# Optimization experiments

Hardware: AMD Instinct MI355X
Metric: run time of the kernel (lower is better)

Reference implementation:

```python
import jax, jax.numpy as jnp
import numpy as np

B, C, H, W = 4, 256, 64, 64
CS = C // 2  # in_channels // scale_factor
EPS = 1e-5


def _conv1x1(x, w, b):
    # x: [B,C,H,W], w: [O,C], b: [O]
    return jnp.einsum('bchw,oc->bohw', x, w) + b[None, :, None, None]


def setup_inputs() -> dict:
    key = jax.random.key(0)
    ks = jax.random.split(key, 12)
    sq, so = 1.0 / np.sqrt(C), 1.0 / np.sqrt(CS)
    inp = {
        'input': jax.random.normal(ks[0], (B, C, H, W), jnp.float32),
        'Wq': jax.random.normal(ks[1], (CS, C), jnp.float32) * sq,
        'bq': jax.random.normal(ks[2], (CS,), jnp.float32) * 0.01,
        'Wk': jax.random.normal(ks[3], (CS, C), jnp.float32) * sq,
        'bk': jax.random.normal(ks[4], (CS,), jnp.float32) * 0.01,
        'Wv': jax.random.normal(ks[5], (CS, C), jnp.float32) * sq,
        'bv': jax.random.normal(ks[6], (CS,), jnp.float32) * 0.01,
        'Wo': jax.random.normal(ks[7], (C, CS), jnp.float32) * so,
        'bo': jax.random.normal(ks[8], (C,), jnp.float32) * 0.01,
        'gamma': 1.0 + 0.1 * jax.random.normal(ks[9], (C,), jnp.float32),
        'beta': 0.1 * jax.random.normal(ks[10], (C,), jnp.float32),
    }
    return inp


def reference(input, Wq, bq, Wk, bk, Wv, bv, Wo, bo, gamma, beta):
    b, c, w, h = input.shape
    n = w * h
    # 1x1-conv projections -> flattened spatial tokens
    q = _conv1x1(input, Wq, bq).reshape(b, CS, n).transpose(0, 2, 1)  # [B,N,CS]
    k = _conv1x1(input, Wk, bk).reshape(b, CS, n)                     # [B,CS,N]
    attn = jax.nn.softmax(jnp.matmul(q, k), axis=-1)                  # [B,N,N]
    v = _conv1x1(input, Wv, bv).reshape(b, CS, n).transpose(0, 2, 1)  # [B,N,CS]
    out = jnp.matmul(attn, v)                                         # [B,N,CS]
    out = out.transpose(0, 2, 1).reshape(b, CS, w, h)
    # output_conv: Conv2d(1x1) -> BatchNorm2d (training-mode batch stats) -> ReLU
    y = _conv1x1(out, Wo, bo)                                         # [B,C,H,W]
    mean = y.mean(axis=(0, 2, 3))
    var = y.var(axis=(0, 2, 3))  # biased, as torch BN normalization
    yn = (y - mean[None, :, None, None]) * jax.lax.rsqrt(var + EPS)[None, :, None, None]
    yn = yn * gamma[None, :, None, None] + beta[None, :, None, None]
    return jax.nn.relu(yn) + input
```

## Files before the change

kernel.cpp:

```cpp
#include <hip/hip_runtime.h>

#define NTOK 4096
#define NCH  256
#define NCS  128
#define NBAT 4

typedef _Float16 f16;
typedef _Float16 f16x8 __attribute__((ext_vector_type(8)));
typedef _Float16 f16x4 __attribute__((ext_vector_type(4)));
typedef __fp16 fp16x2 __attribute__((ext_vector_type(2)));
typedef float f32x16 __attribute__((ext_vector_type(16)));

__device__ __forceinline__ f16 f2h(float f) { return (f16)f; }
__device__ __forceinline__ float h2f(f16 h) { return (float)h; }
__device__ __forceinline__ unsigned short h2s(f16 h) {
  union { f16 h; unsigned short s; } u; u.h = h; return u.s;
}
__device__ __forceinline__ f32x16 mfma32(f16x8 a, f16x8 b, f32x16 c) {
  return __builtin_amdgcn_mfma_f32_32x32x16_f16(a, b, c, 0, 0, 0);
}
__device__ __forceinline__ unsigned pkrtz(float a, float b) {
  union { fp16x2 h; unsigned u; } u;
  u.h = __builtin_amdgcn_cvt_pkrtz(a, b);
  return u.u;
}

__global__ void k_wconv(const float* __restrict__ wq, const float* __restrict__ wk,
                        const float* __restrict__ wv, const float* __restrict__ wo,
                        f16* __restrict__ out) {
  int i = blockIdx.x * 256 + threadIdx.x;
  int seg = i >> 15, off = i & 32767;
  const float* s = (seg == 0) ? wq : (seg == 1) ? wk : (seg == 2) ? wv : wo;
  out[i] = f2h(s[off]);
}

__launch_bounds__(384)
__global__ void k_qkv(const float* __restrict__ x,
                      const f16* __restrict__ wqb, const f16* __restrict__ wkb,
                      const f16* __restrict__ wvb,
                      const float* __restrict__ bq, const float* __restrict__ bk,
                      const float* __restrict__ bv,
                      f16* __restrict__ Qt, f16* __restrict__ Kt, f16* __restrict__ Vc) {
  __shared__ f16 Xs[64][264];
  const int tid = threadIdx.x;
  const int b = blockIdx.y;
  const int t0 = blockIdx.x * 64;
  const int lane = tid & 63, w = tid >> 6;
  {
    for (int cp = w; cp < 128; cp += 6) {
      const float* xp = x + ((size_t)(b * NCH + 2 * cp)) * NTOK + t0 + lane;
      float f0 = xp[0];
      float f1 = xp[NTOK];
      unsigned pk = (unsigned)h2s(f2h(f0)) | ((unsigned)h2s(f2h(f1)) << 16);
      *(unsigned*)&Xs[lane][2 * cp] = pk;
    }
  }
  __syncthreads();
  const int p = w >> 1, th = w & 1;
  const int cc = lane & 31, hi = lane >> 5;
  const f16* wb = (p == 0) ? wqb : (p == 1) ? wkb : wvb;
  const float* bp = (p == 0) ? bq : (p == 1) ? bk : bv;

  f32x16 acc[4];
  #pragma unroll
  for (int nt = 0; nt < 4; nt++)
    #pragma unroll
    for (int i = 0; i < 16; i++) acc[nt][i] = 0.f;
  #pragma unroll
  for (int ks = 0; ks < 16; ks++) {
    f16x8 a = *(const f16x8*)&Xs[th * 32 + cc][ks * 16 + hi * 8];
    #pragma unroll
    for (int nt = 0; nt < 4; nt++) {
      f16x8 bw = *(const f16x8*)(wb + (size_t)(nt * 32 + cc) * NCH + ks * 16 + hi * 8);
      acc[nt] = mfma32(a, bw, acc[nt]);
    }
  }
  if (p < 2) {
    f16* dst = (p == 0) ? Qt : Kt;
    #pragma unroll
    for (int nt = 0; nt < 4; nt++) {
      const int oc = nt * 32 + cc;
      const float bias = bp[oc];
      #pragma unroll
      for (int i = 0; i < 16; i++) {
        int row = (i & 3) + 8 * (i >> 2) + 4 * hi;
        dst[((size_t)b * NTOK + t0 + th * 32 + row) * NCS + oc] = f2h(acc[nt][i] + bias);
      }
    }
  } else {
    #pragma unroll
    for (int nt = 0; nt < 4; nt++) {
      const int oc = nt * 32 + cc;
      const float bias = bp[oc];
      #pragma unroll
      for (int q = 0; q < 4; q++) {
        f16x4 pk;
        #pragma unroll
        for (int j = 0; j < 4; j++) pk[j] = f2h(acc[nt][4 * q + j] + bias);
        *(f16x4*)(Vc + ((size_t)b * NCS + oc) * NTOK + t0 + th * 32 + 8 * q + 4 * hi) = pk;
      }
    }
  }
}

__launch_bounds__(128)
__global__ void k_attn(const f16* __restrict__ Qt, const f16* __restrict__ Kt,
                       const f16* __restrict__ Vc,
                       f16* __restrict__ OP, float* __restrict__ ML, int niter) {
  __shared__ f16 Ks[64][136];
  __shared__ f16 Vs[128][72];
  __shared__ float als[2][32];
  const int tid = threadIdx.x;
  const int b = blockIdx.x & 3, kh = blockIdx.x >> 2, qt = blockIdx.y;
  const int lane = tid & 63, w = tid >> 6, cc = lane & 31, hi = lane >> 5;

  const f16* qp = Qt + ((size_t)b * NTOK + qt * 64 + w * 32 + cc) * NCS + hi * 8;
  f16x8 qf[8];
  #pragma unroll
  for (int ks = 0; ks < 8; ks++) qf[ks] = *(const f16x8*)(qp + ks * 16);

  f32x16 o[4];
  #pragma unroll
  for (int nt = 0; nt < 4; nt++)
    #pragma unroll
    for (int i = 0; i < 16; i++) o[nt][i] = 0.f;
  float m = -1e30f, l = 0.f;

  const int key = tid >> 1, cb = (tid & 1) * 64;
  const int kb0 = kh * niter * 64;

  for (int it = 0; it < niter; it++) {
    const int kb = kb0 + it * 64;
    __syncthreads();
    {
      const f16* kp = Kt + ((size_t)b * NTOK + kb + key) * NCS + cb;
      #pragma unroll
      for (int pp = 0; pp < 8; pp++)
        *(int4*)&Ks[key][cb + pp * 8] = *(const int4*)(kp + pp * 8);
      const f16* vp = Vc + ((size_t)b * NCS + tid) * NTOK + kb;
      #pragma unroll
      for (int pp = 0; pp < 8; pp++)
        *(int4*)&Vs[tid][pp * 8] = *(const int4*)(vp + pp * 8);
    }
    __syncthreads();

    f32x16 s0, s1;
    #pragma unroll
    for (int i = 0; i < 16; i++) { s0[i] = 0.f; s1[i] = 0.f; }
    #pragma unroll
    for (int ks = 0; ks < 8; ks++) {
      f16x8 a0 = *(const f16x8*)&Ks[cc][ks * 16 + hi * 8];
      f16x8 a1 = *(const f16x8*)&Ks[32 + cc][ks * 16 + hi * 8];
      s0 = mfma32(a0, qf[ks], s0);
      s1 = mfma32(a1, qf[ks], s1);
    }
    float pmax = s0[0];
    #pragma unroll
    for (int i = 1; i < 16; i++) pmax = fmaxf(pmax, s0[i]);
    #pragma unroll
    for (int i = 0; i < 16; i++) pmax = fmaxf(pmax, s1[i]);
    pmax = fmaxf(pmax, __shfl_xor(pmax, 32));
    const float mnew = fmaxf(m, pmax);
    const float alpha = __expf(m - mnew);
    float rs = 0.f;
    #pragma unroll
    for (int i = 0; i < 16; i++) { float e = __expf(s0[i] - mnew); s0[i] = e; rs += e; }
    #pragma unroll
    for (int i = 0; i < 16; i++) { float e = __expf(s1[i] - mnew); s1[i] = e; rs += e; }
    rs += __shfl_xor(rs, 32);
    l = l * alpha + rs;
    m = mnew;
    if (hi == 0) als[w][cc] = alpha;

    f16x8 pav[4];
    {
      unsigned Wt[8];
      #pragma unroll
      for (int t = 0; t < 8; t++) Wt[t] = pkrtz(s0[2 * t], s0[2 * t + 1]);
      asm volatile("v_permlane32_swap_b32 %0, %1" : "+v"(Wt[0]), "+v"(Wt[2]));
      asm volatile("v_permlane32_swap_b32 %0, %1" : "+v"(Wt[1]), "+v"(Wt[3]));
      asm volatile("v_permlane32_swap_b32 %0, %1" : "+v"(Wt[4]), "+v"(Wt[6]));
      asm volatile("v_permlane32_swap_b32 %0, %1" : "+v"(Wt[5]), "+v"(Wt[7]));
      union { unsigned u[4]; f16x8 v; } u0, u1;
      #pragma unroll
      for (int t = 0; t < 4; t++) { u0.u[t] = Wt[t]; u1.u[t] = Wt[4 + t]; }
      pav[0] = u0.v; pav[1] = u1.v;
      #pragma unroll
      for (int t = 0; t < 8; t++) Wt[t] = pkrtz(s1[2 * t], s1[2 * t + 1]);
      asm volatile("v_permlane32_swap_b32 %0, %1" : "+v"(Wt[0]), "+v"(Wt[2]));
      asm volatile("v_permlane32_swap_b32 %0, %1" : "+v"(Wt[1]), "+v"(Wt[3]));
      asm volatile("v_permlane32_swap_b32 %0, %1" : "+v"(Wt[4]), "+v"(Wt[6]));
      asm volatile("v_permlane32_swap_b32 %0, %1" : "+v"(Wt[5]), "+v"(Wt[7]));
      #pragma unroll
      for (int t = 0; t < 4; t++) { u0.u[t] = Wt[t]; u1.u[t] = Wt[4 + t]; }
      pav[2] = u0.v; pav[3] = u1.v;
    }

    float ar[16];
    #pragma unroll
    for (int i = 0; i < 16; i++) ar[i] = als[w][(i & 3) + 8 * (i >> 2) + 4 * hi];
    #pragma unroll
    for (int nt = 0; nt < 4; nt++)
      #pragma unroll
      for (int i = 0; i < 16; i++) o[nt][i] *= ar[i];
    #pragma unroll
    for (int ks = 0; ks < 4; ks++) {
      #pragma unroll
      for (int nt = 0; nt < 4; nt++) {
        f16x8 bv = *(const f16x8*)&Vs[nt * 32 + cc][ks * 16 + hi * 8];
        o[nt] = mfma32(pav[ks], bv, o[nt]);
      }
    }
  }
  const size_t obase = (((size_t)kh * NBAT + b) * NTOK + qt * 64 + w * 32);
  if (hi == 0) {
    const size_t mi = obase + cc;
    ML[mi * 2] = m; ML[mi * 2 + 1] = l;
  }
  #pragma unroll
  for (int nt = 0; nt < 4; nt++)
    #pragma unroll
    for (int i = 0; i < 16; i++) {
      int row = (i & 3) + 8 * (i >> 2) + 4 * hi;
      OP[(obase + row) * NCS + nt * 32 + cc] = f2h(o[nt][i]);
    }
}

template <int S>
__global__ void k_comb(const f16* __restrict__ OP, const float* __restrict__ ML,
                       f16* __restrict__ Oa) {
  const int gid = blockIdx.x * 256 + threadIdx.x;
  const int tok = gid >> 4, dg = (gid & 15) * 8;
  const int b = tok >> 12, tn = tok & 4095;
  float mv[S], lv[S];
  float mm = -1e30f;
  #pragma unroll
  for (int s = 0; s < S; s++) {
    const size_t idx = (((size_t)s * NBAT + b) * NTOK + tn);
    mv[s] = ML[idx * 2]; lv[s] = ML[idx * 2 + 1];
    mm = fmaxf(mm, mv[s]);
  }
  float den = 0.f, wsc[S];
  #pragma unroll
  for (int s = 0; s < S; s++) { wsc[s] = __expf(mv[s] - mm); den += wsc[s] * lv[s]; }
  const float inv = 1.f / den;
  float oacc[8];
  #pragma unroll
  for (int j = 0; j < 8; j++) oacc[j] = 0.f;
  #pragma unroll
  for (int s = 0; s < S; s++) {
    const size_t idx = (((size_t)s * NBAT + b) * NTOK + tn);
    int4 v = *(const int4*)(OP + idx * NCS + dg);
    const f16* a = (const f16*)&v;
    #pragma unroll
    for (int j = 0; j < 8; j++) oacc[j] += wsc[s] * h2f(a[j]);
  }
  f16x8 vv;
  #pragma unroll
  for (int j = 0; j < 8; j++) vv[j] = f2h(oacc[j] * inv);
  *(f16x8*)(Oa + ((size_t)b * NTOK + tn) * NCS + dg) = vv;
}

__launch_bounds__(256)
__global__ void k_out(const f16* __restrict__ Oa, const f16* __restrict__ wob,
                      const float* __restrict__ bo,
                      f16* __restrict__ Yb, float* __restrict__ Psum) {
  __shared__ f16 Es[256][72];
  const int tid = threadIdx.x;
  const int b = blockIdx.y, tt = blockIdx.x, t0 = tt * 64;
  const int lane = tid & 63, w = tid >> 6, cc = lane & 31, hi = lane >> 5;
  const int th = w >> 1, oh = w & 1;
  const f16* op = Oa + ((size_t)b * NTOK + t0 + th * 32 + cc) * NCS + hi * 8;
  f16x8 af[8];
  #pragma unroll
  for (int ks = 0; ks < 8; ks++) af[ks] = *(const f16x8*)(op + ks * 16);
  f32x16 acc[4];
  #pragma unroll
  for (int nt = 0; nt < 4; nt++)
    #pragma unroll
    for (int i = 0; i < 16; i++) acc[nt][i] = 0.f;
  #pragma unroll
  for (int ks = 0; ks < 8; ks++)
    #pragma unroll
    for (int nt = 0; nt < 4; nt++) {
      f16x8 bw = *(const f16x8*)(wob + (size_t)(oh * 128 + nt * 32 + cc) * NCS + ks * 16 + hi * 8);
      acc[nt] = mfma32(af[ks], bw, acc[nt]);
    }
  #pragma unroll
  for (int nt = 0; nt < 4; nt++) {
    const int co = oh * 128 + nt * 32 + cc;
    const float bias = bo[co];
    float s = 0.f, sq = 0.f;
    #pragma unroll
    for (int i = 0; i < 16; i++) {
      float v = acc[nt][i] + bias;
      acc[nt][i] = v; s += v; sq += v * v;
    }
    s += __shfl_xor(s, 32); sq += __shfl_xor(sq, 32);
    if (hi == 0) {
      const size_t pi = ((size_t)(b * 64 + tt) * 2 + th) * NCH + co;
      Psum[pi * 2] = s; Psum[pi * 2 + 1] = sq;
    }
    #pragma unroll
    for (int q = 0; q < 4; q++) {
      f16x4 pk;
      #pragma unroll
      for (int j = 0; j < 4; j++) pk[j] = f2h(acc[nt][4 * q + j]);
      *(f16x4*)&Es[co][th * 32 + q * 8 + hi * 4] = pk;
    }
  }
  __syncthreads();
  {
    const f16* er = &Es[tid][0];
    f16* yp = Yb + ((size_t)b * NCH + tid) * NTOK + t0;
    #pragma unroll
    for (int p = 0; p < 8; p++)
      *(int4*)(yp + p * 8) = *(const int4*)(er + p * 8);
  }
}

__global__ void k_stats(const float* __restrict__ Psum, float* __restrict__ St) {
  const int ch = blockIdx.x, tid = threadIdx.x;
  float s = 0.f, sq = 0.f;
  for (int i = tid; i < 512; i += 128) {
    s  += Psum[((size_t)i * NCH + ch) * 2];
    sq += Psum[((size_t)i * NCH + ch) * 2 + 1];
  }
  #pragma unroll
  for (int off = 32; off >= 1; off >>= 1) { s += __shfl_down(s, off); sq += __shfl_down(sq, off); }
  __shared__ float red[4];
  if ((tid & 63) == 0) { red[(tid >> 6) * 2] = s; red[(tid >> 6) * 2 + 1] = sq; }
  __syncthreads();
  if (tid == 0) {
    s = red[0] + red[2]; sq = red[1] + red[3];
    const float mean = s * (1.f / 16384.f);
    const float var = sq * (1.f / 16384.f) - mean * mean;
    St[ch * 2] = mean;
    St[ch * 2 + 1] = 1.f / sqrtf(var + 1e-5f);
  }
}

__global__ void k_final(const f16* __restrict__ Yb, const float* __restrict__ x,
                        const float* __restrict__ St, const float* __restrict__ gamma,
                        const float* __restrict__ beta, float* __restrict__ out) {
  const size_t i = ((size_t)blockIdx.x * 256 + threadIdx.x) * 8;
  const int ch = (int)((i >> 12) & 255);
  const float mean = St[ch * 2], rstd = St[ch * 2 + 1];
  const float sc = gamma[ch] * rstd;
  const float sh = beta[ch] - mean * sc;
  int4 yv = *(const int4*)(Yb + i);
  const f16* ys = (const f16*)&yv;
  const float4 x0 = *(const float4*)(x + i);
  const float4 x1 = *(const float4*)(x + i + 4);
  float4 o0, o1;
  o0.x = fmaxf(h2f(ys[0]) * sc + sh, 0.f) + x0.x;
  o0.y = fmaxf(h2f(ys[1]) * sc + sh, 0.f) + x0.y;
  o0.z = fmaxf(h2f(ys[2]) * sc + sh, 0.f) + x0.z;
  o0.w = fmaxf(h2f(ys[3]) * sc + sh, 0.f) + x0.w;
  o1.x = fmaxf(h2f(ys[4]) * sc + sh, 0.f) + x1.x;
  o1.y = fmaxf(h2f(ys[5]) * sc + sh, 0.f) + x1.y;
  o1.z = fmaxf(h2f(ys[6]) * sc + sh, 0.f) + x1.z;
  o1.w = fmaxf(h2f(ys[7]) * sc + sh, 0.f) + x1.w;
  *(float4*)(out + i) = o0;
  *(float4*)(out + i + 4) = o1;
}

extern "C" void kernel_launch(void* const* d_in, const int* in_sizes, int n_in,
                              void* d_out, int out_size, void* d_ws, size_t ws_size,
                              hipStream_t stream) {
  const float* x     = (const float*)d_in[0];
  const float* Wq    = (const float*)d_in[1];
  const float* bq    = (const float*)d_in[2];
  const float* Wk    = (const float*)d_in[3];
  const float* bk    = (const float*)d_in[4];
  const float* Wv    = (const float*)d_in[5];
  const float* bv    = (const float*)d_in[6];
  const float* Wo    = (const float*)d_in[7];
  const float* bo    = (const float*)d_in[8];
  const float* gamma = (const float*)d_in[9];
  const float* beta  = (const float*)d_in[10];
  float* out = (float*)d_out;
  char* ws = (char*)d_ws;

  const size_t OFF_W  = 0;
  const size_t OFF_QT = 262144;
  const size_t OFF_KT = OFF_QT + 4194304;
  const size_t OFF_VC = OFF_KT + 4194304;
  const size_t OFF_OP = OFF_VC + 4194304;
  const size_t opsz8 = (size_t)8 * NBAT * NTOK * NCS * 2;
  const size_t mlsz8 = (size_t)8 * NBAT * NTOK * 2 * 4;
  const size_t need8 = OFF_OP + opsz8 + mlsz8 + 1048576 + 4096;
  const int SPLIT = (ws_size >= need8) ? 8 : 4;
  const size_t opsz = (size_t)SPLIT * NBAT * NTOK * NCS * 2;
  const size_t mlsz = (size_t)SPLIT * NBAT * NTOK * 2 * 4;
  const size_t OFF_ML = OFF_OP + opsz;
  const size_t OFF_PS = OFF_ML + mlsz;
  const size_t OFF_ST = OFF_PS + 1048576;

  f16* wqb = (f16*)(ws + OFF_W);
  f16* wkb = (f16*)(ws + OFF_W + 65536);
  f16* wvb = (f16*)(ws + OFF_W + 131072);
  f16* wob = (f16*)(ws + OFF_W + 196608);
  f16* Qt  = (f16*)(ws + OFF_QT);
  f16* Kt  = (f16*)(ws + OFF_KT);
  f16* Vc  = (f16*)(ws + OFF_VC);
  f16* OP  = (f16*)(ws + OFF_OP);
  float* ML = (float*)(ws + OFF_ML);
  float* Psum = (float*)(ws + OFF_PS);
  float* St   = (float*)(ws + OFF_ST);
  f16* Yb = (f16*)(ws + OFF_QT);
  f16* Oa = (f16*)(ws + OFF_VC);

  k_wconv<<<512, 256, 0, stream>>>(Wq, Wk, Wv, Wo, wqb);
  k_qkv<<<dim3(64, 4), 384, 0, stream>>>(x, wqb, wkb, wvb, bq, bk, bv, Qt, Kt, Vc);
  k_attn<<<dim3(4 * SPLIT, 64), 128, 0, stream>>>(Qt, Kt, Vc, OP, ML, 64 / SPLIT);
  if (SPLIT == 8) k_comb<8><<<1024, 256, 0, stream>>>(OP, ML, Oa);
  else            k_comb<4><<<1024, 256, 0, stream>>>(OP, ML, Oa);
  k_out<<<dim3(64, 4), 256, 0, stream>>>(Oa, wob, bo, Yb, Psum);
  k_stats<<<256, 128, 0, stream>>>(Psum, St);
  k_final<<<2048, 256, 0, stream>>>(Yb, x, St, gamma, beta, out);
}
```

Measured before the change: 235.9 us.

## Widen attention blocks to 128 queries, skip rescale when max unchanged, retile QKV

The attention kernel now runs 4 waves per block covering 128 query rows. Each K/V tile loaded into shared memory is reused by twice as many queries, which halves global K/V traffic per query, and a launch bound requests more resident blocks. The online softmax uses a tree max reduction and, when no lane's running max grows (checked wave-wide with __all), skips the alpha computation and the rescale of the output accumulators. The QKV projection kernel is retiled to 32 tokens per block with 12 waves, each wave owning one 32-channel output tile, giving more blocks and less register pressure at the cost of redundant weight reads.

Result: slower. 446.3 us (+89.2%).

```diff
diff --git a/kernel.cpp b/kernel.cpp
--- a/kernel.cpp
+++ b/kernel.cpp
@@ -34,87 +34,73 @@
   out[i] = f2h(s[off]);
 }
 
-__launch_bounds__(384)
+__launch_bounds__(768)
 __global__ void k_qkv(const float* __restrict__ x,
                       const f16* __restrict__ wqb, const f16* __restrict__ wkb,
                       const f16* __restrict__ wvb,
                       const float* __restrict__ bq, const float* __restrict__ bk,
                       const float* __restrict__ bv,
                       f16* __restrict__ Qt, f16* __restrict__ Kt, f16* __restrict__ Vc) {
-  __shared__ f16 Xs[64][264];
+  __shared__ f16 Xs[32][264];
   const int tid = threadIdx.x;
   const int b = blockIdx.y;
-  const int t0 = blockIdx.x * 64;
+  const int t0 = blockIdx.x * 32;
+  for (int idx = tid; idx < 4096; idx += 768) {
+    const int tok = idx & 31, cp = idx >> 5;
+    const float* xp = x + ((size_t)(b * NCH + 2 * cp)) * NTOK + t0 + tok;
+    float f0 = xp[0];
+    float f1 = xp[NTOK];
+    unsigned pk = (unsigned)h2s(f2h(f0)) | ((unsigned)h2s(f2h(f1)) << 16);
+    *(unsigned*)&Xs[tok][2 * cp] = pk;
+  }
+  __syncthreads();
   const int lane = tid & 63, w = tid >> 6;
-  {
-    for (int cp = w; cp < 128; cp += 6) {
-      const float* xp = x + ((size_t)(b * NCH + 2 * cp)) * NTOK + t0 + lane;
-      float f0 = xp[0];
-      float f1 = xp[NTOK];
-      unsigned pk = (unsigned)h2s(f2h(f0)) | ((unsigned)h2s(f2h(f1)) << 16);
-      *(unsigned*)&Xs[lane][2 * cp] = pk;
-    }
-  }
-  __syncthreads();
-  const int p = w >> 1, th = w & 1;
+  const int p = w >> 2, nt = w & 3;
   const int cc = lane & 31, hi = lane >> 5;
   const f16* wb = (p == 0) ? wqb : (p == 1) ? wkb : wvb;
   const float* bp = (p == 0) ? bq : (p == 1) ? bk : bv;
 
-  f32x16 acc[4];
-  #pragma unroll
-  for (int nt = 0; nt < 4; nt++)
-    #pragma unroll
-    for (int i = 0; i < 16; i++) acc[nt][i] = 0.f;
+  f32x16 acc;
+  #pragma unroll
+  for (int i = 0; i < 16; i++) acc[i] = 0.f;
   #pragma unroll
   for (int ks = 0; ks < 16; ks++) {
-    f16x8 a = *(const f16x8*)&Xs[th * 32 + cc][ks * 16 + hi * 8];
-    #pragma unroll
-    for (int nt = 0; nt < 4; nt++) {
-      f16x8 bw = *(const f16x8*)(wb + (size_t)(nt * 32 + cc) * NCH + ks * 16 + hi * 8);
-      acc[nt] = mfma32(a, bw, acc[nt]);
-    }
-  }
+    f16x8 a = *(const f16x8*)&Xs[cc][ks * 16 + hi * 8];
+    f16x8 bw = *(const f16x8*)(wb + (size_t)(nt * 32 + cc) * NCH + ks * 16 + hi * 8);
+    acc = mfma32(a, bw, acc);
+  }
+  const int oc = nt * 32 + cc;
+  const float bias = bp[oc];
   if (p < 2) {
     f16* dst = (p == 0) ? Qt : Kt;
     #pragma unroll
-    for (int nt = 0; nt < 4; nt++) {
-      const int oc = nt * 32 + cc;
-      const float bias = bp[oc];
-      #pragma unroll
-      for (int i = 0; i < 16; i++) {
-        int row = (i & 3) + 8 * (i >> 2) + 4 * hi;
-        dst[((size_t)b * NTOK + t0 + th * 32 + row) * NCS + oc] = f2h(acc[nt][i] + bias);
-      }
+    for (int i = 0; i < 16; i++) {
+      int row = (i & 3) + 8 * (i >> 2) + 4 * hi;
+      dst[((size_t)b * NTOK + t0 + row) * NCS + oc] = f2h(acc[i] + bias);
     }
   } else {
     #pragma unroll
-    for (int nt = 0; nt < 4; nt++) {
-      const int oc = nt * 32 + cc;
-      const float bias = bp[oc];
-      #pragma unroll
-      for (int q = 0; q < 4; q++) {
-        f16x4 pk;
-        #pragma unroll
-        for (int j = 0; j < 4; j++) pk[j] = f2h(acc[nt][4 * q + j] + bias);
-        *(f16x4*)(Vc + ((size_t)b * NCS + oc) * NTOK + t0 + th * 32 + 8 * q + 4 * hi) = pk;
-      }
-    }
-  }
-}
-
-__launch_bounds__(128)
+    for (int q = 0; q < 4; q++) {
+      f16x4 pk;
+      #pragma unroll
+      for (int j = 0; j < 4; j++) pk[j] = f2h(acc[4 * q + j] + bias);
+      *(f16x4*)(Vc + ((size_t)b * NCS + oc) * NTOK + t0 + 8 * q + 4 * hi) = pk;
+    }
+  }
+}
+
+__launch_bounds__(256, 4)
 __global__ void k_attn(const f16* __restrict__ Qt, const f16* __restrict__ Kt,
                        const f16* __restrict__ Vc,
                        f16* __restrict__ OP, float* __restrict__ ML, int niter) {
   __shared__ f16 Ks[64][136];
   __shared__ f16 Vs[128][72];
-  __shared__ float als[2][32];
+  __shared__ float als[4][32];
   const int tid = threadIdx.x;
   const int b = blockIdx.x & 3, kh = blockIdx.x >> 2, qt = blockIdx.y;
   const int lane = tid & 63, w = tid >> 6, cc = lane & 31, hi = lane >> 5;
 
-  const f16* qp = Qt + ((size_t)b * NTOK + qt * 64 + w * 32 + cc) * NCS + hi * 8;
+  const f16* qp = Qt + ((size_t)b * NTOK + qt * 128 + w * 32 + cc) * NCS + hi * 8;
   f16x8 qf[8];
   #pragma unroll
   for (int ks = 0; ks < 8; ks++) qf[ks] = *(const f16x8*)(qp + ks * 16);
@@ -126,21 +112,22 @@
     for (int i = 0; i < 16; i++) o[nt][i] = 0.f;
   float m = -1e30f, l = 0.f;
 
-  const int key = tid >> 1, cb = (tid & 1) * 64;
+  const int kkey = tid >> 2, kcb = (tid & 3) * 32;
+  const int vd = tid >> 1, vh = (tid & 1) * 32;
   const int kb0 = kh * niter * 64;
 
   for (int it = 0; it < niter; it++) {
     const int kb = kb0 + it * 64;
     __syncthreads();
     {
-      const f16* kp = Kt + ((size_t)b * NTOK + kb + key) * NCS + cb;
-      #pragma unroll
-      for (int pp = 0; pp < 8; pp++)
-        *(int4*)&Ks[key][cb + pp * 8] = *(const int4*)(kp + pp * 8);
-      const f16* vp = Vc + ((size_t)b * NCS + tid) * NTOK + kb;
-      #pragma unroll
-      for (int pp = 0; pp < 8; pp++)
-        *(int4*)&Vs[tid][pp * 8] = *(const int4*)(vp + pp * 8);
+      const f16* kp = Kt + ((size_t)b * NTOK + kb + kkey) * NCS + kcb;
+      #pragma unroll
+      for (int pp = 0; pp < 4; pp++)
+        *(int4*)&Ks[kkey][kcb + pp * 8] = *(const int4*)(kp + pp * 8);
+      const f16* vp = Vc + ((size_t)b * NCS + vd) * NTOK + kb + vh;
+      #pragma unroll
+      for (int pp = 0; pp < 4; pp++)
+        *(int4*)&Vs[vd][vh + pp * 8] = *(const int4*)(vp + pp * 8);
     }
     __syncthreads();
 
@@ -154,55 +141,68 @@
       s0 = mfma32(a0, qf[ks], s0);
       s1 = mfma32(a1, qf[ks], s1);
     }
-    float pmax = s0[0];
-    #pragma unroll
-    for (int i = 1; i < 16; i++) pmax = fmaxf(pmax, s0[i]);
-    #pragma unroll
-    for (int i = 0; i < 16; i++) pmax = fmaxf(pmax, s1[i]);
-    pmax = fmaxf(pmax, __shfl_xor(pmax, 32));
-    const float mnew = fmaxf(m, pmax);
-    const float alpha = __expf(m - mnew);
-    float rs = 0.f;
-    #pragma unroll
-    for (int i = 0; i < 16; i++) { float e = __expf(s0[i] - mnew); s0[i] = e; rs += e; }
-    #pragma unroll
-    for (int i = 0; i < 16; i++) { float e = __expf(s1[i] - mnew); s1[i] = e; rs += e; }
-    rs += __shfl_xor(rs, 32);
-    l = l * alpha + rs;
-    m = mnew;
-    if (hi == 0) als[w][cc] = alpha;
+    float t[16];
+    #pragma unroll
+    for (int i = 0; i < 16; i++) t[i] = fmaxf(s0[i], s1[i]);
+    #pragma unroll
+    for (int st = 8; st >= 1; st >>= 1)
+      #pragma unroll
+      for (int i = 0; i < st; i++) t[i] = fmaxf(t[i], t[i + st]);
+    const float pmax = fmaxf(t[0], __shfl_xor(t[0], 32));
+
+    if (__all(pmax <= m)) {
+      float rs = 0.f;
+      #pragma unroll
+      for (int i = 0; i < 16; i++) { float e = __expf(s0[i] - m); s0[i] = e; rs += e; }
+      #pragma unroll
+      for (int i = 0; i < 16; i++) { float e = __expf(s1[i] - m); s1[i] = e; rs += e; }
+      rs += __shfl_xor(rs, 32);
+      l += rs;
+    } else {
+      const float mnew = fmaxf(m, pmax);
+      const float alpha = __expf(m - mnew);
+      float rs = 0.f;
+      #pragma unroll
+      for (int i = 0; i < 16; i++) { float e = __expf(s0[i] - mnew); s0[i] = e; rs += e; }
+      #pragma unroll
+      for (int i = 0; i < 16; i++) { float e = __expf(s1[i] - mnew); s1[i] = e; rs += e; }
+      rs += __shfl_xor(rs, 32);
+      l = l * alpha + rs;
+      m = mnew;
+      if (hi == 0) als[w][cc] = alpha;
+      float ar[16];
+      #pragma unroll
+      for (int i = 0; i < 16; i++) ar[i] = als[w][(i & 3) + 8 * (i >> 2) + 4 * hi];
+      #pragma unroll
+      for (int nt = 0; nt < 4; nt++)
+        #pragma unroll
+        for (int i = 0; i < 16; i++) o[nt][i] *= ar[i];
+    }
 
     f16x8 pav[4];
     {
       unsigned Wt[8];
       #pragma unroll
-      for (int t = 0; t < 8; t++) Wt[t] = pkrtz(s0[2 * t], s0[2 * t + 1]);
+      for (int t2 = 0; t2 < 8; t2++) Wt[t2] = pkrtz(s0[2 * t2], s0[2 * t2 + 1]);
       asm volatile("v_permlane32_swap_b32 %0, %1" : "+v"(Wt[0]), "+v"(Wt[2]));
       asm volatile("v_permlane32_swap_b32 %0, %1" : "+v"(Wt[1]), "+v"(Wt[3]));
       asm volatile("v_permlane32_swap_b32 %0, %1" : "+v"(Wt[4]), "+v"(Wt[6]));
       asm volatile("v_permlane32_swap_b32 %0, %1" : "+v"(Wt[5]), "+v"(Wt[7]));
       union { unsigned u[4]; f16x8 v; } u0, u1;
       #pragma unroll
-      for (int t = 0; t < 4; t++) { u0.u[t] = Wt[t]; u1.u[t] = Wt[4 + t]; }
+      for (int t2 = 0; t2 < 4; t2++) { u0.u[t2] = Wt[t2]; u1.u[t2] = Wt[4 + t2]; }
       pav[0] = u0.v; pav[1] = u1.v;
       #pragma unroll
-      for (int t = 0; t < 8; t++) Wt[t] = pkrtz(s1[2 * t], s1[2 * t + 1]);
+      for (int t2 = 0; t2 < 8; t2++) Wt[t2] = pkrtz(s1[2 * t2], s1[2 * t2 + 1]);
       asm volatile("v_permlane32_swap_b32 %0, %1" : "+v"(Wt[0]), "+v"(Wt[2]));
       asm volatile("v_permlane32_swap_b32 %0, %1" : "+v"(Wt[1]), "+v"(Wt[3]));
       asm volatile("v_permlane32_swap_b32 %0, %1" : "+v"(Wt[4]), "+v"(Wt[6]));
       asm volatile("v_permlane32_swap_b32 %0, %1" : "+v"(Wt[5]), "+v"(Wt[7]));
       #pragma unroll
-      for (int t = 0; t < 4; t++) { u0.u[t] = Wt[t]; u1.u[t] = Wt[4 + t]; }
+      for (int t2 = 0; t2 < 4; t2++) { u0.u[t2] = Wt[t2]; u1.u[t2] = Wt[4 + t2]; }
       pav[2] = u0.v; pav[3] = u1.v;
     }
 
-    float ar[16];
-    #pragma unroll
-    for (int i = 0; i < 16; i++) ar[i] = als[w][(i & 3) + 8 * (i >> 2) + 4 * hi];
-    #pragma unroll
-    for (int nt = 0; nt < 4; nt++)
-      #pragma unroll
-      for (int i = 0; i < 16; i++) o[nt][i] *= ar[i];
     #pragma unroll
     for (int ks = 0; ks < 4; ks++) {
       #pragma unroll
@@ -212,7 +212,7 @@
       }
     }
   }
-  const size_t obase = (((size_t)kh * NBAT + b) * NTOK + qt * 64 + w * 32);
+  const size_t obase = (((size_t)kh * NBAT + b) * NTOK + qt * 128 + w * 32);
   if (hi == 0) {
     const size_t mi = obase + cc;
     ML[mi * 2] = m; ML[mi * 2 + 1] = l;
@@ -412,8 +412,8 @@
   f16* Oa = (f16*)(ws + OFF_VC);
 
   k_wconv<<<512, 256, 0, stream>>>(Wq, Wk, Wv, Wo, wqb);
-  k_qkv<<<dim3(64, 4), 384, 0, stream>>>(x, wqb, wkb, wvb, bq, bk, bv, Qt, Kt, Vc);
-  k_attn<<<dim3(4 * SPLIT, 64), 128, 0, stream>>>(Qt, Kt, Vc, OP, ML, 64 / SPLIT);
+  k_qkv<<<dim3(128, 4), 768, 0, stream>>>(x, wqb, wkb, wvb, bq, bk, bv, Qt, Kt, Vc);
+  k_attn<<<dim3(4 * SPLIT, 32), 256, 0, stream>>>(Qt, Kt, Vc, OP, ML, 64 / SPLIT);
   if (SPLIT == 8) k_comb<8><<<1024, 256, 0, stream>>>(OP, ML, Oa);
   else            k_comb<4><<<1024, 256, 0, stream>>>(OP, ML, Oa);
   k_out<<<dim3(64, 4), 256, 0, stream>>>(Oa, wob, bo, Yb, Psum);
```
